# Performance work log

Measured on AMD Instinct MI355X. Metric: run time of the kernel, lower is better.

## Reference

```python
import jax, jax.numpy as jnp
import numpy as np

V, E, DIN, DOUT, NREL2 = 80000, 640000, 128, 128, 500
EPS = 1e-5


def ccorr(a, b):
    # circular cross-correlation: irfft(conj(rfft(a)) * rfft(b))
    fa = jnp.fft.rfft(a, axis=-1)
    fb = jnp.fft.rfft(b, axis=-1)
    return jnp.fft.irfft(jnp.conj(fa) * fb, n=a.shape[-1], axis=-1)


def setup_inputs() -> dict:
    key = jax.random.key(0)
    ks = jax.random.split(key, 14)
    s = 0.1  # xavier-ish scale
    return {
        'x': jax.random.normal(ks[0], (V, DIN), jnp.float32),
        'x_t': jnp.zeros((V, 16), jnp.float32),
        'x_i': jnp.zeros((V, 16), jnp.float32),
        'x_n': jnp.zeros((V, 16), jnp.float32),
        'rel_repr': jax.random.normal(ks[1], (NREL2, DIN), jnp.float32) * s,
        'edge_norm': jax.random.uniform(ks[2], (E,), jnp.float32),
        'in_w': jax.random.normal(ks[3], (DIN, DOUT), jnp.float32) * s,
        'out_w': jax.random.normal(ks[4], (DIN, DOUT), jnp.float32) * s,
        'loop_w': jax.random.normal(ks[5], (DIN, DOUT), jnp.float32) * s,
        'w_rel': jax.random.normal(ks[6], (DIN, DOUT), jnp.float32) * s,
        'loop_rel': jax.random.normal(ks[7], (1, DIN), jnp.float32) * s,
        'attn_w': jax.random.normal(ks[8], (3 * DIN,), jnp.float32) * 0.05,
        'bias': jnp.zeros((DOUT,), jnp.float32),
        'src': jax.random.randint(ks[9], (E,), 0, V),
        'dst': jax.random.randint(ks[10], (E,), 0, V),
        'edge_type': jax.random.randint(ks[11], (E,), 0, NREL2),
    }


def reference(x, x_t, x_i, x_n, rel_repr, edge_norm, in_w, out_w, loop_w,
              w_rel, loop_rel, attn_w, bias, src, dst, edge_type):
    nV = x.shape[0]
    nE = src.shape[0]
    rel = rel_repr  # rel_wt is None (num_base <= 0)

    src_h = x[src]              # [E, din] gather
    dst_h = x[dst]              # [E, din]
    rel_h = rel[edge_type]      # [E, din]

    # edge attention: attn_fc(cat[src,rel,dst]) == split-weight form
    w_s, w_r, w_d = jnp.split(attn_w, 3)
    e = jax.nn.leaky_relu(src_h @ w_s + rel_h @ w_r + dst_h @ w_d, 0.01)  # [E]

    # message: FFT composition then half in_w / half out_w
    edh = ccorr(src_h, rel_h)                                  # [E, din]
    half = nE // 2
    msg = jnp.concatenate([edh[:half] @ in_w, edh[half:] @ out_w], axis=0)
    msg = jax.nn.softmax(msg, axis=1)  # F.softmax default dim=1 for 2D
    msg = msg * edge_norm[:, None]

    # segment softmax of e over destination-node mailboxes
    emax = jax.ops.segment_max(e, dst, num_segments=nV)
    emax = jnp.where(jnp.isfinite(emax), emax, 0.0)
    ee = jnp.exp(e - emax[dst])
    esum = jax.ops.segment_sum(ee, dst, num_segments=nV)
    alpha = ee / jnp.where(esum[dst] > 0, esum[dst], 1.0)      # [E]

    h = jax.ops.segment_sum(alpha[:, None] * msg, dst, num_segments=nV) / 3.0

    # self-loop branch
    loop = ccorr(x, jnp.broadcast_to(loop_rel, x.shape)) @ loop_w / 3.0

    out = h + loop + bias
    # BatchNorm1d, training mode, affine weight=1 bias=0 (default init)
    mean = out.mean(axis=0)
    var = out.var(axis=0)
    out = (out - mean) / jnp.sqrt(var + EPS)
    return out, rel @ w_rel
```

## Files before the change

kernel.cpp:

```cpp
#include <hip/hip_runtime.h>

#define V 80000
#define E 640000
#define D 128
#define NREL 500
#define HALF (E/2)
#define NGROUP 1000
#define EP (E + NGROUP * 32)
#define NBLK_D ((V + 1023) / 1024)
#define NREP 160
#define SLABLOG 12
#define SLAB 4096
#define NSLAB ((E + SLAB - 1) / SLAB)

typedef __attribute__((ext_vector_type(8))) short s8v;
typedef __attribute__((ext_vector_type(4))) float f4v;
typedef __attribute__((ext_vector_type(4))) int i4v;
typedef unsigned long long u64;

__device__ __forceinline__ unsigned short f2bf(float f) {
  unsigned u = __float_as_uint(f);
  return (unsigned short)((u + 0x7fffu + ((u >> 16) & 1u)) >> 16);
}

__global__ void k_init(u64* packed, int* hist, uint4* edat) {
  int i = blockIdx.x * 256 + threadIdx.x;
  if (i < V) packed[i] = 0ull;
  if (i < NGROUP * NREP) hist[i] = 0;
  if (i < EP) { uint4 r; r.x = 0; r.y = 0xFFFFFFFFu; r.z = 0; r.w = 0; edat[i] = r; }
}

__global__ void k_prep(const float* __restrict__ rel, const float* __restrict__ w_rel,
                       const float* __restrict__ attn_w, const float* __restrict__ loop_rel,
                       const float* __restrict__ loop_w, const float* __restrict__ in_w,
                       const float* __restrict__ out_w, float* __restrict__ out1,
                       float* __restrict__ rw, unsigned short* __restrict__ relb,
                       unsigned short* __restrict__ mltb, unsigned short* __restrict__ wtb) {
  int b = blockIdx.x, n = threadIdx.x;
  if (b < NREL) {
    __shared__ float rs[D];
    __shared__ float red[D];
    float rv = rel[b * D + n];
    rs[n] = rv;
    relb[b * D + n] = f2bf(rv);
    red[n] = rv * attn_w[D + n];
    __syncthreads();
    float acc = 0.f;
    #pragma unroll 8
    for (int j = 0; j < D; ++j) acc += rs[j] * w_rel[j * D + n];
    out1[b * D + n] = acc;
    if (n == 0) {
      float s = 0.f;
      for (int j = 0; j < D; ++j) s += red[j];
      rw[b] = s;
    }
  } else if (b < NREL + D) {
    int j = b - NREL;
    __shared__ float ls[2 * D];
    ls[n] = loop_rel[n]; ls[n + D] = loop_rel[n];
    __syncthreads();
    float acc = 0.f;
    #pragma unroll 8
    for (int k = 0; k < D; ++k) acc += ls[j + k] * loop_w[k * D + n];
    mltb[n * D + j] = f2bf(acc);
  } else {
    int bw = b - NREL - D;
    int h = bw >> 7, n2 = bw & 127;
    const float* W = h ? out_w : in_w;
    wtb[h * 16384 + n2 * D + n] = f2bf(W[n * D + n2]);
  }
}

__global__ void k_xbproj(const float* __restrict__ x, const float* __restrict__ attn_w,
                         unsigned* __restrict__ xb32, float* __restrict__ sxw,
                         float* __restrict__ dxw) {
  int tid = threadIdx.x;
  int wid = tid >> 6, lane = tid & 63;
  float ws0 = attn_w[2 * lane], ws1 = attn_w[2 * lane + 1];
  float wd0 = attn_w[256 + 2 * lane], wd1 = attn_w[256 + 2 * lane + 1];
  for (int v = blockIdx.x * 4 + wid; v < V; v += 2048 * 4) {
    float2 xv = *(const float2*)&x[(size_t)v * D + 2 * lane];
    float ps = xv.x * ws0 + xv.y * ws1;
    float pd = xv.x * wd0 + xv.y * wd1;
    #pragma unroll
    for (int off = 32; off; off >>= 1) { ps += __shfl_xor(ps, off); pd += __shfl_xor(pd, off); }
    if (lane == 0) { sxw[v] = ps; dxw[v] = pd; }
    xb32[(size_t)v * 64 + lane] = (unsigned)f2bf(xv.x) | ((unsigned)f2bf(xv.y) << 16);
  }
}

__global__ __launch_bounds__(256) void k_mbt2(const unsigned short* __restrict__ relb,
    const unsigned short* __restrict__ wtb, unsigned short* __restrict__ mbt) {
  __shared__ unsigned short relp[256];
  __shared__ unsigned short Wl[D * D];
  int g = blockIdx.x, tid = threadIdx.x;
  int t = (g >= NREL) ? g - NREL : g;
  const unsigned short* wt = wtb + (g >= NREL ? 16384 : 0);
  relp[tid] = relb[t * D + (tid & 127)];
  #pragma unroll
  for (int i = 0; i < 8; ++i) {
    int idx = tid + i * 256;
    int n = idx >> 4, kc = idx & 15;
    *(uint4*)((char*)Wl + n * 256 + ((kc ^ (n & 7)) << 4)) = *(const uint4*)(wt + n * D + kc * 8);
  }
  __syncthreads();
  int wid = tid >> 6, ln = tid & 15, hi = (tid & 63) >> 4;
  s8v af[2][4];
  #pragma unroll
  for (int m = 0; m < 2; ++m) {
    int j = wid * 32 + m * 16 + ln;
    #pragma unroll
    for (int ks = 0; ks < 4; ++ks) {
      int o = j + ks * 32 + hi * 8;
      s8v a;
      #pragma unroll
      for (int i = 0; i < 8; ++i) a[i] = (short)relp[o + i];
      af[m][ks] = a;
    }
  }
  f4v acc[2][8];
  #pragma unroll
  for (int m = 0; m < 2; ++m)
    #pragma unroll
    for (int nn = 0; nn < 8; ++nn) acc[m][nn] = (f4v){0.f, 0.f, 0.f, 0.f};
  #pragma unroll
  for (int ks = 0; ks < 4; ++ks) {
    #pragma unroll
    for (int nn = 0; nn < 8; ++nn) {
      int n2 = nn * 16 + ln;
      int kc = (ks * 4 + hi) ^ (n2 & 7);
      s8v b = *(const s8v*)((const char*)Wl + n2 * 256 + (kc << 4));
      #pragma unroll
      for (int m = 0; m < 2; ++m)
        acc[m][nn] = __builtin_amdgcn_mfma_f32_16x16x32_bf16(af[m][ks], b, acc[m][nn], 0, 0, 0);
    }
  }
  size_t gb = (size_t)g * (D * D);
  #pragma unroll
  for (int m = 0; m < 2; ++m)
    #pragma unroll
    for (int nn = 0; nn < 8; ++nn) {
      int jb = wid * 32 + m * 16 + hi * 4;
      u64 pk = (u64)f2bf(acc[m][nn][0])
        | ((u64)f2bf(acc[m][nn][1]) << 16)
        | ((u64)f2bf(acc[m][nn][2]) << 32)
        | ((u64)f2bf(acc[m][nn][3]) << 48);
      *(u64*)&mbt[gb + (size_t)(nn * 16 + ln) * D + jb] = pk;
    }
}

__global__ __launch_bounds__(256) void k_lgemm(const unsigned short* __restrict__ xb,
    const unsigned short* __restrict__ mltb, const float* __restrict__ bias,
    float* __restrict__ out0) {
  __shared__ unsigned short Wl[D * D];
  int tid = threadIdx.x;
  #pragma unroll
  for (int i = 0; i < 8; ++i) {
    int idx = tid + i * 256;
    int n = idx >> 4, kc = idx & 15;
    *(uint4*)((char*)Wl + n * 256 + ((kc ^ (n & 7)) << 4)) = *(const uint4*)(mltb + n * D + kc * 8);
  }
  __syncthreads();
  int wid = tid >> 6, ln = tid & 15, hi = (tid & 63) >> 4;
  int rbase = blockIdx.x * 128 + wid * 32;
  s8v af[2][4];
  #pragma unroll
  for (int m = 0; m < 2; ++m)
    #pragma unroll
    for (int ks = 0; ks < 4; ++ks)
      af[m][ks] = *(const s8v*)(xb + (size_t)(rbase + m * 16 + ln) * D + ks * 32 + hi * 8);
  f4v acc[2][8];
  #pragma unroll
  for (int m = 0; m < 2; ++m)
    #pragma unroll
    for (int nn = 0; nn < 8; ++nn) acc[m][nn] = (f4v){0.f, 0.f, 0.f, 0.f};
  #pragma unroll
  for (int ks = 0; ks < 4; ++ks) {
    #pragma unroll
    for (int nn = 0; nn < 8; ++nn) {
      int n2 = nn * 16 + ln;
      int kc = (ks * 4 + hi) ^ (n2 & 7);
      s8v b = *(const s8v*)((const char*)Wl + n2 * 256 + (kc << 4));
      #pragma unroll
      for (int m = 0; m < 2; ++m)
        acc[m][nn] = __builtin_amdgcn_mfma_f32_16x16x32_bf16(af[m][ks], b, acc[m][nn], 0, 0, 0);
    }
  }
  float bcol[8];
  #pragma unroll
  for (int nn = 0; nn < 8; ++nn) bcol[nn] = bias[nn * 16 + ln];
  #pragma unroll
  for (int m = 0; m < 2; ++m)
    #pragma unroll
    for (int nn = 0; nn < 8; ++nn)
      #pragma unroll
      for (int r = 0; r < 4; ++r)
        out0[(size_t)(rbase + m * 16 + hi * 4 + r) * D + nn * 16 + ln] =
            acc[m][nn][r] * (1.f / 3.f) + bcol[nn];
}

__global__ __launch_bounds__(512) void k_edge(const int* __restrict__ src,
                       const int* __restrict__ dst,
                       const int* __restrict__ et, const float* __restrict__ sxw,
                       const float* __restrict__ dxw, const float* __restrict__ rw,
                       float* __restrict__ evals, u64* __restrict__ packed,
                       int* __restrict__ hist, unsigned short* __restrict__ drank,
                       unsigned short* __restrict__ grank) {
  __shared__ int lhist[NGROUP];
  int r = blockIdx.x, tid = threadIdx.x;
  for (int t = tid; t < NGROUP; t += 512) lhist[t] = 0;
  __syncthreads();
  #pragma unroll
  for (int c = 0; c < 8; ++c) {
    int i = r * SLAB + c * 512 + tid;
    if (i < E) {
      int d = dst[i];
      float ev = sxw[src[i]] + rw[et[i]] + dxw[d];
      ev = ev >= 0.f ? ev : 0.01f * ev;
      float xv = __expf(ev);
      evals[i] = xv;
      u64 inc = (1ull << 48) + (u64)(xv * 65536.f + 0.5f);
      u64 old = atomicAdd(&packed[d], inc);
      drank[i] = (unsigned short)(old >> 48);
      int g = et[i] + ((i >= HALF) ? NREL : 0);
      int gr = atomicAdd(&lhist[g], 1);
      grank[i] = (unsigned short)gr;
    }
  }
  __syncthreads();
  for (int t = tid; t < NGROUP; t += 512) hist[t * NREP + r] = lhist[t];
}

__global__ void k_dscan1(const u64* __restrict__ packed, float* __restrict__ esum,
                         int* __restrict__ dloc, int* __restrict__ dtot,
                         const int* __restrict__ hist, int* __restrict__ cnt,
                         int* __restrict__ poffs, int* __restrict__ repbase) {
  __shared__ int tmp[1024];
  int t = threadIdx.x;
  if (blockIdx.x == NBLK_D) {
    int c = 0;
    if (t < NGROUP) {
      for (int r = 0; r < NREP; ++r) c += hist[t * NREP + r];
      cnt[t] = c;
    }
    int pc = (c + 31) & ~31;
    tmp[t] = pc;
    __syncthreads();
    #pragma unroll
    for (int off = 1; off < 1024; off <<= 1) {
      int v = (t >= off) ? tmp[t - off] : 0;
      __syncthreads();
      tmp[t] += v;
      __syncthreads();
    }
    int po = tmp[t] - pc;
    poffs[t] = po;
    if (t < NGROUP) {
      int running = po;
      for (int r = 0; r < NREP; ++r) {
        repbase[t * NREP + r] = running;
        running += hist[t * NREP + r];
      }
    }
    return;
  }
  int i = blockIdx.x * 1024 + t;
  int v = 0;
  if (i < V) {
    u64 q = packed[i];
    esum[i] = (float)(q & 0xFFFFFFFFFFFFull) * (1.f / 65536.f);
    v = (int)(q >> 48);
  }
  tmp[t] = v;
  __syncthreads();
  #pragma unroll
  for (int off = 1; off < 1024; off <<= 1) {
    int u = (t >= off) ? tmp[t - off] : 0;
    __syncthreads();
    tmp[t] += u;
    __syncthreads();
  }
  if (i < V) dloc[i] = tmp[t] - v;
  if (t == 1023) dtot[blockIdx.x] = tmp[t];
}

__global__ void k_dscan3(const int* __restrict__ dloc, const int* __restrict__ dtot,
                         int* __restrict__ doffs) {
  __shared__ int sh[128];
  int t = threadIdx.x;
  if (t < 128) sh[t] = (t < NBLK_D) ? dtot[t] : 0;
  __syncthreads();
  #pragma unroll
  for (int off = 1; off < 128; off <<= 1) {
    int v = (t >= off && t < 128) ? sh[t - off] : 0;
    __syncthreads();
    if (t < 128) sh[t] += v;
    __syncthreads();
  }
  int bo = (blockIdx.x == 0) ? 0 : sh[blockIdx.x - 1];
  int i = blockIdx.x * 1024 + t;
  if (i < V) doffs[i] = dloc[i] + bo;
  if (i == 0) doffs[V] = E;
}

__global__ void k_scatter(const int* __restrict__ src, const int* __restrict__ dst,
                          const int* __restrict__ et, const float* __restrict__ ee,
                          const float* __restrict__ esum, const float* __restrict__ enorm,
                          const int* __restrict__ repbase, const int* __restrict__ doffs,
                          const unsigned short* __restrict__ drank,
                          const unsigned short* __restrict__ grank,
                          uint4* __restrict__ edat) {
  int i = blockIdx.x * 256 + threadIdx.x;
  if (i >= E) return;
  int g = et[i] + ((i >= HALF) ? NREL : 0);
  int r = i >> SLABLOG;
  int pos = repbase[g * NREP + r] + (int)grank[i];
  int d = dst[i];
  uint4 rec;
  rec.x = (unsigned)src[i];
  rec.y = (unsigned)(doffs[d] + (int)drank[i]);
  rec.z = __float_as_uint(ee[i] / esum[d] * enorm[i] * (1.f / 3.f));
  rec.w = 0;
  edat[pos] = rec;
}

__global__ __launch_bounds__(256) void k_msg3(const unsigned short* __restrict__ xb,
    const unsigned short* __restrict__ mbt, const int* __restrict__ cnt,
    const int* __restrict__ poffs, const uint4* __restrict__ edat,
    const int* __restrict__ doffs, int loNode, int hiNode,
    unsigned short* __restrict__ msgb) {
  __shared__ uint4 Blds4[(D * 272) / 16];
  unsigned char* Bldsb = (unsigned char*)Blds4;
  int g = blockIdx.x >> 1, half = blockIdx.x & 1;
  int c = cnt[g];
  if (c == 0) return;
  int tid = threadIdx.x;
  const uint4* Mg = (const uint4*)(mbt + (size_t)g * (D * D));
  #pragma unroll
  for (int i = 0; i < 8; ++i) {
    int idx = tid + i * 256;
    int row = idx >> 4, col = (idx & 15) * 16;
    Blds4[(row * 272 + col) >> 4] = Mg[idx];
  }
  __syncthreads();
  int b1 = doffs[loNode];
  int b2 = doffs[hiNode];
  int wid = tid >> 6, ln = tid & 15, hi = (tid & 63) >> 4;
  int base0 = poffs[g];
  int nch = (c + 15) >> 4;
  int ch = half * 4 + wid;
  uint4 recp;
  s8v afp[4];
  if (ch < nch) {
    recp = edat[base0 + ch * 16 + ln];
    const unsigned short* xr = xb + (size_t)recp.x * D + hi * 8;
    #pragma unroll
    for (int ks = 0; ks < 4; ++ks) afp[ks] = *(const s8v*)(xr + ks * 32);
  }
  for (; ch < nch; ch += 8) {
    uint4 recc = recp;
    int nc2 = ch + 8;
    if (nc2 < nch) recp = edat[base0 + nc2 * 16 + ln];
    s8v afc[4];
    #pragma unroll
    for (int ks = 0; ks < 4; ++ks) afc[ks] = afp[ks];
    f4v acc[8];
    #pragma unroll
    for (int n = 0; n < 8; ++n) acc[n] = (f4v){0.f, 0.f, 0.f, 0.f};
    #pragma unroll
    for (int ks = 0; ks < 4; ++ks) {
      #pragma unroll
      for (int n = 0; n < 8; ++n) {
        int row = n * 16 + ln;
        s8v bf = *(const s8v*)(Bldsb + row * 272 + ks * 64 + hi * 16);
        acc[n] = __builtin_amdgcn_mfma_f32_16x16x32_bf16(afc[ks], bf, acc[n], 0, 0, 0);
      }
    }
    if (nc2 < nch) {
      const unsigned short* xr = xb + (size_t)recp.x * D + hi * 8;
      #pragma unroll
      for (int ks = 0; ks < 4; ++ks) afp[ks] = *(const s8v*)(xr + ks * 32);
    }
    f4v sum = (f4v){0.f, 0.f, 0.f, 0.f};
    #pragma unroll
    for (int n = 0; n < 8; ++n)
      #pragma unroll
      for (int j = 0; j < 4; ++j) {
        float e = __expf(acc[n][j]);
        acc[n][j] = e;
        sum[j] += e;
      }
    #pragma unroll
    for (int off = 1; off < 16; off <<= 1)
      #pragma unroll
      for (int j = 0; j < 4; ++j) sum[j] += __shfl_xor(sum[j], off);
    #pragma unroll
    for (int j = 0; j < 4; ++j) {
      int dpos = __shfl((int)recc.y, hi * 4 + j, 16);
      if (dpos >= b1 && dpos < b2) {
        float cf = __uint_as_float(__shfl((int)recc.z, hi * 4 + j, 16));
        size_t rowb = (size_t)(dpos - b1) * D;
        float s = cf / sum[j];
        unsigned q0 = (unsigned)f2bf(acc[0][j] * s) | ((unsigned)f2bf(acc[1][j] * s) << 16);
        unsigned q1 = (unsigned)f2bf(acc[2][j] * s) | ((unsigned)f2bf(acc[3][j] * s) << 16);
        unsigned q2 = (unsigned)f2bf(acc[4][j] * s) | ((unsigned)f2bf(acc[5][j] * s) << 16);
        unsigned q3 = (unsigned)f2bf(acc[6][j] * s) | ((unsigned)f2bf(acc[7][j] * s) << 16);
        uint4 qv; qv.x = q0; qv.y = q1; qv.z = q2; qv.w = q3;
        *(uint4*)&msgb[rowb + ln * 8] = qv;
      }
    }
  }
}

__global__ void k_sum(const unsigned short* __restrict__ msgb, const int* __restrict__ doffs,
                      float* __restrict__ out0, int loNode, int hiNode) {
  int tid = threadIdx.x;
  int wid = tid >> 6, lane = tid & 63;
  int sub = lane >> 4, ln = lane & 15;
  int d = loNode + blockIdx.x * 16 + wid * 4 + sub;
  if (d >= hiNode) return;
  int b1 = doffs[loNode];
  int s0 = doffs[d];
  int len = doffs[d + 1] - s0;
  const unsigned short* mp = msgb + (size_t)(s0 - b1) * D + ln * 8;
  float a[8];
  #pragma unroll
  for (int n = 0; n < 8; ++n) a[n] = 0.f;
  for (int r = 0; r < len; ++r) {
    uint4 q = *(const uint4*)(mp + (size_t)r * D);
    a[0] += __uint_as_float(q.x << 16);
    a[1] += __uint_as_float(q.x & 0xffff0000u);
    a[2] += __uint_as_float(q.y << 16);
    a[3] += __uint_as_float(q.y & 0xffff0000u);
    a[4] += __uint_as_float(q.z << 16);
    a[5] += __uint_as_float(q.z & 0xffff0000u);
    a[6] += __uint_as_float(q.w << 16);
    a[7] += __uint_as_float(q.w & 0xffff0000u);
  }
  float* orow = out0 + (size_t)d * D + ln;
  #pragma unroll
  for (int n = 0; n < 8; ++n) orow[n * 16] += a[n];
}

__global__ void k_bn1(const float* __restrict__ out0, float* __restrict__ part) {
  __shared__ float sh[256];
  int tid = threadIdx.x;
  int col = tid & 127, r = tid >> 7;
  float s = 0.f, q = 0.f;
  for (int v = blockIdx.x * 2 + r; v < V; v += 1024) {
    float val = out0[(size_t)v * D + col];
    s += val; q += val * val;
  }
  sh[tid] = s;
  __syncthreads();
  if (r == 0) part[blockIdx.x * 256 + col] = sh[col] + sh[col + 128];
  __syncthreads();
  sh[tid] = q;
  __syncthreads();
  if (r == 0) part[blockIdx.x * 256 + 128 + col] = sh[col] + sh[col + 128];
}

__global__ void k_bn2(const float* __restrict__ part, float* __restrict__ mrs) {
  __shared__ float sh[256];
  int t = threadIdx.x;
  float s = 0.f;
  for (int b = 0; b < 512; ++b) s += part[b * 256 + t];
  sh[t] = s;
  __syncthreads();
  if (t < 128) {
    float mean = sh[t] * (1.f / V);
    float var = sh[128 + t] * (1.f / V) - mean * mean;
    mrs[t] = mean;
    mrs[128 + t] = rsqrtf(var + 1e-5f);
  }
}

__global__ void k_bn_norm(float* __restrict__ out0, const float* __restrict__ mrs) {
  int i = blockIdx.x * 256 + threadIdx.x;
  if (i >= V * D) return;
  int c = i & 127;
  out0[i] = (out0[i] - mrs[c]) * mrs[128 + c];
}

extern "C" void kernel_launch(void* const* d_in, const int* in_sizes, int n_in,
                              void* d_out, int out_size, void* d_ws, size_t ws_size,
                              hipStream_t stream) {
  const float* x        = (const float*)d_in[0];
  const float* rel      = (const float*)d_in[4];
  const float* enorm    = (const float*)d_in[5];
  const float* in_w     = (const float*)d_in[6];
  const float* out_w    = (const float*)d_in[7];
  const float* loop_w   = (const float*)d_in[8];
  const float* w_rel    = (const float*)d_in[9];
  const float* loop_rel = (const float*)d_in[10];
  const float* attn_w   = (const float*)d_in[11];
  const float* bias     = (const float*)d_in[12];
  const int* src = (const int*)d_in[13];
  const int* dst = (const int*)d_in[14];
  const int* et  = (const int*)d_in[15];

  float* out0 = (float*)d_out;
  float* out1 = out0 + (size_t)V * D;

  float* base = (float*)d_ws;
  size_t off = 0;
  float* sxw = base + off;      off += V;
  float* dxw = base + off;      off += V;
  float* esum = base + off;     off += V;
  float* evals = base + off;    off += E;
  float* rw = base + off;       off += 512;
  float* part = base + off;     off += 512 * 256;
  float* mrs = base + off;      off += 256;
  int* cnt = (int*)(base + off);   off += 1024;
  int* poffs = (int*)(base + off); off += 1024;
  int* hist = (int*)(base + off);     off += NGROUP * NREP;
  int* repbase = (int*)(base + off);  off += NGROUP * NREP;
  u64* packed = (u64*)(base + off);   off += 2 * V;
  int* dloc = (int*)(base + off);  off += V;
  int* doffs = (int*)(base + off); off += V + 2;
  int* dtot = (int*)(base + off);  off += 128;
  unsigned short* drank = (unsigned short*)(base + off); off += E / 2;
  unsigned short* grank = (unsigned short*)(base + off); off += E / 2;
  uint4* edat = (uint4*)(base + off); off += (size_t)4 * EP;
  unsigned short* mltb = (unsigned short*)(base + off); off += D * D / 2;
  unsigned short* relb = (unsigned short*)(base + off); off += NREL * D / 2;
  unsigned short* wtb  = (unsigned short*)(base + off); off += 2 * D * D / 2;
  unsigned short* xb   = (unsigned short*)(base + off); off += (size_t)V * D / 2;
  unsigned short* mbt  = (unsigned short*)(base + off); off += (size_t)NGROUP * D * D / 2;
  unsigned short* msgb = (unsigned short*)(base + off);

  size_t availF = (ws_size / 4 > off) ? (ws_size / 4 - off) : 0;
  int ns = 1;
  if ((size_t)EP * (D / 2) > availF) {
    ns = 2;
    while (ns < 64 && (size_t)(E / ns + 16384) * (D / 2) > availF) ns *= 2;
  }

  k_init<<<(EP + 255) / 256, 256, 0, stream>>>(packed, hist, edat);
  k_prep<<<NREL + D + 256, 128, 0, stream>>>(rel, w_rel, attn_w, loop_rel, loop_w,
                                             in_w, out_w, out1, rw, relb, mltb, wtb);
  k_xbproj<<<2048, 256, 0, stream>>>(x, attn_w, (unsigned*)xb, sxw, dxw);
  k_mbt2<<<NGROUP, 256, 0, stream>>>(relb, wtb, mbt);
  k_lgemm<<<V / 128, 256, 0, stream>>>(xb, mltb, bias, out0);
  k_edge<<<NSLAB, 512, 0, stream>>>(src, dst, et, sxw, dxw, rw,
                                    evals, packed, hist, drank, grank);
  k_dscan1<<<NBLK_D + 1, 1024, 0, stream>>>(packed, esum, dloc, dtot,
                                            hist, cnt, poffs, repbase);
  k_dscan3<<<NBLK_D, 1024, 0, stream>>>(dloc, dtot, doffs);
  k_scatter<<<(E + 255) / 256, 256, 0, stream>>>(src, dst, et, evals, esum, enorm,
                                                 repbase, doffs, drank, grank, edat);
  int Vs = V / ns;
  for (int s = 0; s < ns; ++s) {
    int lo = s * Vs, hi = (s == ns - 1) ? V : (s + 1) * Vs;
    k_msg3<<<NGROUP * 2, 256, 0, stream>>>(xb, mbt, cnt, poffs, edat,
                                           doffs, lo, hi, msgb);
    k_sum<<<(Vs + 15) / 16, 256, 0, stream>>>(msgb, doffs, out0, lo, hi);
  }
  k_bn1<<<512, 256, 0, stream>>>(out0, part);
  k_bn2<<<1, 256, 0, stream>>>(part, mrs);
  k_bn_norm<<<(V * D + 255) / 256, 256, 0, stream>>>(out0, mrs);
}
```

Measured before the change: 377.0 us.

## Fuse BatchNorm statistics into k_sum, halve edge slabs, one block per group

Batch-norm column sums and sums of squares are now accumulated inside k_sum with shared-memory atomics and written to per-block partials. This removes the separate k_bn1 pass that re-read the whole output, and a two-stage reduction replaces k_bn2. Edge slabs shrink from 4096 to 2048 edges, giving more k_edge blocks and doubling the replica count. k_msg3 now launches one block per group instead of two, which cuts B-matrix reloads but lowers parallelism. The shared atomics on only 256 addresses may contend, and each partial block must be zeroed in init.

```diff
diff --git a/kernel.cpp b/kernel.cpp
--- a/kernel.cpp
+++ b/kernel.cpp
@@ -8,10 +8,12 @@
 #define NGROUP 1000
 #define EP (E + NGROUP * 32)
 #define NBLK_D ((V + 1023) / 1024)
-#define NREP 160
-#define SLABLOG 12
-#define SLAB 4096
+#define NREP 320
+#define SLABLOG 11
+#define SLAB 2048
 #define NSLAB ((E + SLAB - 1) / SLAB)
+#define NSUMBLK ((V + 15) / 16)
+#define NPART (NSUMBLK * 256)
 
 typedef __attribute__((ext_vector_type(8))) short s8v;
 typedef __attribute__((ext_vector_type(4))) float f4v;
@@ -23,11 +25,12 @@
   return (unsigned short)((u + 0x7fffu + ((u >> 16) & 1u)) >> 16);
 }
 
-__global__ void k_init(u64* packed, int* hist, uint4* edat) {
+__global__ void k_init(u64* packed, int* hist, uint4* edat, float* part) {
   int i = blockIdx.x * 256 + threadIdx.x;
   if (i < V) packed[i] = 0ull;
   if (i < NGROUP * NREP) hist[i] = 0;
   if (i < EP) { uint4 r; r.x = 0; r.y = 0xFFFFFFFFu; r.z = 0; r.w = 0; edat[i] = r; }
+  if (i < NPART) part[i] = 0.f;
 }
 
 __global__ void k_prep(const float* __restrict__ rel, const float* __restrict__ w_rel,
@@ -211,7 +214,7 @@
   for (int t = tid; t < NGROUP; t += 512) lhist[t] = 0;
   __syncthreads();
   #pragma unroll
-  for (int c = 0; c < 8; ++c) {
+  for (int c = 0; c < 4; ++c) {
     int i = r * SLAB + c * 512 + tid;
     if (i < E) {
       int d = dst[i];
@@ -331,7 +334,7 @@
     unsigned short* __restrict__ msgb) {
   __shared__ uint4 Blds4[(D * 272) / 16];
   unsigned char* Bldsb = (unsigned char*)Blds4;
-  int g = blockIdx.x >> 1, half = blockIdx.x & 1;
+  int g = blockIdx.x;
   int c = cnt[g];
   if (c == 0) return;
   int tid = threadIdx.x;
@@ -348,7 +351,7 @@
   int wid = tid >> 6, ln = tid & 15, hi = (tid & 63) >> 4;
   int base0 = poffs[g];
   int nch = (c + 15) >> 4;
-  int ch = half * 4 + wid;
+  int ch = wid;
   uint4 recp;
   s8v afp[4];
   if (ch < nch) {
@@ -357,9 +360,9 @@
     #pragma unroll
     for (int ks = 0; ks < 4; ++ks) afp[ks] = *(const s8v*)(xr + ks * 32);
   }
-  for (; ch < nch; ch += 8) {
+  for (; ch < nch; ch += 4) {
     uint4 recc = recp;
-    int nc2 = ch + 8;
+    int nc2 = ch + 4;
     if (nc2 < nch) recp = edat[base0 + nc2 * 16 + ln];
     s8v afc[4];
     #pragma unroll
@@ -413,58 +416,62 @@
 }
 
 __global__ void k_sum(const unsigned short* __restrict__ msgb, const int* __restrict__ doffs,
-                      float* __restrict__ out0, int loNode, int hiNode) {
+                      float* __restrict__ out0, float* __restrict__ part,
+                      int loNode, int hiNode) {
+  __shared__ float bnp[2 * D];
   int tid = threadIdx.x;
+  for (int t = tid; t < 2 * D; t += 256) bnp[t] = 0.f;
+  __syncthreads();
   int wid = tid >> 6, lane = tid & 63;
   int sub = lane >> 4, ln = lane & 15;
   int d = loNode + blockIdx.x * 16 + wid * 4 + sub;
-  if (d >= hiNode) return;
-  int b1 = doffs[loNode];
-  int s0 = doffs[d];
-  int len = doffs[d + 1] - s0;
-  const unsigned short* mp = msgb + (size_t)(s0 - b1) * D + ln * 8;
-  float a[8];
-  #pragma unroll
-  for (int n = 0; n < 8; ++n) a[n] = 0.f;
-  for (int r = 0; r < len; ++r) {
-    uint4 q = *(const uint4*)(mp + (size_t)r * D);
-    a[0] += __uint_as_float(q.x << 16);
-    a[1] += __uint_as_float(q.x & 0xffff0000u);
-    a[2] += __uint_as_float(q.y << 16);
-    a[3] += __uint_as_float(q.y & 0xffff0000u);
-    a[4] += __uint_as_float(q.z << 16);
-    a[5] += __uint_as_float(q.z & 0xffff0000u);
-    a[6] += __uint_as_float(q.w << 16);
-    a[7] += __uint_as_float(q.w & 0xffff0000u);
-  }
-  float* orow = out0 + (size_t)d * D + ln;
-  #pragma unroll
-  for (int n = 0; n < 8; ++n) orow[n * 16] += a[n];
-}
-
-__global__ void k_bn1(const float* __restrict__ out0, float* __restrict__ part) {
-  __shared__ float sh[256];
-  int tid = threadIdx.x;
-  int col = tid & 127, r = tid >> 7;
-  float s = 0.f, q = 0.f;
-  for (int v = blockIdx.x * 2 + r; v < V; v += 1024) {
-    float val = out0[(size_t)v * D + col];
-    s += val; q += val * val;
-  }
-  sh[tid] = s;
-  __syncthreads();
-  if (r == 0) part[blockIdx.x * 256 + col] = sh[col] + sh[col + 128];
-  __syncthreads();
-  sh[tid] = q;
-  __syncthreads();
-  if (r == 0) part[blockIdx.x * 256 + 128 + col] = sh[col] + sh[col + 128];
-}
-
-__global__ void k_bn2(const float* __restrict__ part, float* __restrict__ mrs) {
+  if (d < hiNode) {
+    int b1 = doffs[loNode];
+    int s0 = doffs[d];
+    int len = doffs[d + 1] - s0;
+    const unsigned short* mp = msgb + (size_t)(s0 - b1) * D + ln * 8;
+    float a[8];
+    #pragma unroll
+    for (int n = 0; n < 8; ++n) a[n] = 0.f;
+    for (int r = 0; r < len; ++r) {
+      uint4 q = *(const uint4*)(mp + (size_t)r * D);
+      a[0] += __uint_as_float(q.x << 16);
+      a[1] += __uint_as_float(q.x & 0xffff0000u);
+      a[2] += __uint_as_float(q.y << 16);
+      a[3] += __uint_as_float(q.y & 0xffff0000u);
+      a[4] += __uint_as_float(q.z << 16);
+      a[5] += __uint_as_float(q.z & 0xffff0000u);
+      a[6] += __uint_as_float(q.w << 16);
+      a[7] += __uint_as_float(q.w & 0xffff0000u);
+    }
+    float* orow = out0 + (size_t)d * D + ln;
+    #pragma unroll
+    for (int n = 0; n < 8; ++n) {
+      float v = orow[n * 16] + a[n];
+      orow[n * 16] = v;
+      int col = n * 16 + ln;
+      atomicAdd(&bnp[col], v);
+      atomicAdd(&bnp[D + col], v * v);
+    }
+  }
+  __syncthreads();
+  float* pb = part + (size_t)blockIdx.x * 256;
+  for (int t = tid; t < 2 * D; t += 256) pb[t] += bnp[t];
+}
+
+__global__ void k_bn2a(const float* __restrict__ part, float* __restrict__ part2) {
+  int t = threadIdx.x, b = blockIdx.x;
+  int r0 = b * 50;
+  float s = 0.f;
+  for (int r = r0; r < r0 + 50 && r < NSUMBLK; ++r) s += part[(size_t)r * 256 + t];
+  part2[b * 256 + t] = s;
+}
+
+__global__ void k_bn2b(const float* __restrict__ part2, float* __restrict__ mrs) {
   __shared__ float sh[256];
   int t = threadIdx.x;
   float s = 0.f;
-  for (int b = 0; b < 512; ++b) s += part[b * 256 + t];
+  for (int b = 0; b < 100; ++b) s += part2[b * 256 + t];
   sh[t] = s;
   __syncthreads();
   if (t < 128) {
@@ -509,7 +516,8 @@
   float* esum = base + off;     off += V;
   float* evals = base + off;    off += E;
   float* rw = base + off;       off += 512;
-  float* part = base + off;     off += 512 * 256;
+  float* part = base + off;     off += (size_t)NPART;
+  float* part2 = base + off;    off += 100 * 256;
   float* mrs = base + off;      off += 256;
   int* cnt = (int*)(base + off);   off += 1024;
   int* poffs = (int*)(base + off); off += 1024;
@@ -536,7 +544,8 @@
     while (ns < 64 && (size_t)(E / ns + 16384) * (D / 2) > availF) ns *= 2;
   }
 
-  k_init<<<(EP + 255) / 256, 256, 0, stream>>>(packed, hist, edat);
+  int initGrid = (NPART > EP ? NPART : EP);
+  k_init<<<(initGrid + 255) / 256, 256, 0, stream>>>(packed, hist, edat, part);
   k_prep<<<NREL + D + 256, 128, 0, stream>>>(rel, w_rel, attn_w, loop_rel, loop_w,
                                              in_w, out_w, out1, rw, relb, mltb, wtb);
   k_xbproj<<<2048, 256, 0, stream>>>(x, attn_w, (unsigned*)xb, sxw, dxw);
@@ -552,11 +561,11 @@
   int Vs = V / ns;
   for (int s = 0; s < ns; ++s) {
     int lo = s * Vs, hi = (s == ns - 1) ? V : (s + 1) * Vs;
-    k_msg3<<<NGROUP * 2, 256, 0, stream>>>(xb, mbt, cnt, poffs, edat,
-                                           doffs, lo, hi, msgb);
-    k_sum<<<(Vs + 15) / 16, 256, 0, stream>>>(msgb, doffs, out0, lo, hi);
-  }
-  k_bn1<<<512, 256, 0, stream>>>(out0, part);
-  k_bn2<<<1, 256, 0, stream>>>(part, mrs);
+    k_msg3<<<NGROUP, 256, 0, stream>>>(xb, mbt, cnt, poffs, edat,
+                                       doffs, lo, hi, msgb);
+    k_sum<<<(Vs + 15) / 16, 256, 0, stream>>>(msgb, doffs, out0, part, lo, hi);
+  }
+  k_bn2a<<<100, 256, 0, stream>>>(part, part2);
+  k_bn2b<<<1, 256, 0, stream>>>(part2, mrs);
   k_bn_norm<<<(V * D + 255) / 256, 256, 0, stream>>>(out0, mrs);
 }
```

After: 515.7 us. +36.8%, slower.
